# Kernel tuning notes

Measured on AMD Instinct MI355X. Metric: run time of the kernel, lower is better.

## Reference

```python
import jax, jax.numpy as jnp
import numpy as np

NUM_SAMPLES = 1024


def _cdist(a, b):
    # a, b: (n, 3) -> (n, n) pairwise euclidean distances (torch.cdist p=2)
    d2 = jnp.sum((a[:, None, :] - b[None, :, :]) ** 2, axis=-1)
    return jnp.sqrt(jnp.maximum(d2, 0.0))


def _greedy_match_cost(cost):
    # Greedy sequential matching: repeatedly take the global argmin over
    # still-unmatched rows/cols, accumulate its cost, eliminate row+col.
    n = cost.shape[0]

    def step(carry, _):
        row_mask, col_mask, loss = carry
        valid = row_mask[:, None] & col_mask[None, :]
        masked = jnp.where(valid, cost, jnp.inf)
        idx = jnp.argmin(masked)  # row-major first-min == torch's min(dim=1)+argmin tiebreak
        r = idx // n
        c = idx % n
        loss = loss + cost[r, c]
        return (row_mask.at[r].set(False), col_mask.at[c].set(False), loss), None

    init = (jnp.ones((n,), dtype=bool), jnp.ones((n,), dtype=bool), jnp.float32(0.0))
    (_, _, loss), _ = jax.lax.scan(step, init, None, length=n)
    return loss / n


def setup_inputs() -> dict:
    key = jax.random.key(0)
    k1, k2, k3 = jax.random.split(key, 3)
    B, N, n = 8, 4096, NUM_SAMPLES
    S1 = jax.random.normal(k1, (B, N, 3), dtype=jnp.float32)
    S2 = jax.random.normal(k2, (B, N, 3), dtype=jnp.float32)
    # torch.randperm(N)[:n] per batch element: without-replacement sampling
    perm_keys = jax.random.split(k3, B)
    indices = jax.vmap(lambda k: jax.random.permutation(k, N)[:n])(perm_keys).astype(jnp.int32)
    return {"S1": S1, "S2": S2, "indices": indices}


def reference(S1, S2, indices):
    # sample the same indices from both sets, per batch (matches original loop)
    s1 = jnp.take_along_axis(S1, indices[:, :, None], axis=1)  # (B, n, 3)
    s2 = jnp.take_along_axis(S2, indices[:, :, None], axis=1)  # (B, n, 3)
    cost = jax.vmap(_cdist)(s1, s2)  # (B, n, n)
    losses = jax.vmap(_greedy_match_cost)(cost)  # (B,)
    return jnp.mean(losses)
```

## Files before the change

### kernel.cpp

```cpp
#include <hip/hip_runtime.h>
#include <stdint.h>

#define BATCH 8
#define NPTS 4096
#define NS 1024
#define KD 6

typedef unsigned long long u64;
typedef unsigned int u32;
typedef unsigned short u16;
typedef unsigned char u8;

#define DEADV (~0ull)
#define QNANB 0x7FC00000u
#define INFB  0x7F800000u

__device__ __forceinline__ float pdist3(float ax, float ay, float az,
                                        float bx, float by, float bz) {
    float dx = ax - bx, dy = ay - by, dz = az - bz;
    float d2 = __fmaf_rn(dz, dz, __fmaf_rn(dy, dy, dx * dx));
    return __fsqrt_rn(d2);
}

__device__ __forceinline__ u64 packv(float d, u32 row, u32 col) {
    return ((u64)__float_as_uint(d) << 20) | ((u64)row << 10) | (u64)col;
}

__device__ __forceinline__ u64 u64min2(u64 a, u64 b) { return a < b ? a : b; }

__device__ __forceinline__ u64 tree16(const u64* p) {
    u64 a0 = u64min2(p[0], p[1]),   a1 = u64min2(p[2], p[3]);
    u64 a2 = u64min2(p[4], p[5]),   a3 = u64min2(p[6], p[7]);
    u64 a4 = u64min2(p[8], p[9]),   a5 = u64min2(p[10], p[11]);
    u64 a6 = u64min2(p[12], p[13]), a7 = u64min2(p[14], p[15]);
    u64 b0 = u64min2(a0, a1), b1 = u64min2(a2, a3);
    u64 b2 = u64min2(a4, a5), b3 = u64min2(a6, a7);
    return u64min2(u64min2(b0, b1), u64min2(b2, b3));
}

template<int CTRL>
__device__ __forceinline__ u64 dpp_min_step(u64 m) {
    u32 lo = (u32)m, hi = (u32)(m >> 32);
    u32 olo = (u32)__builtin_amdgcn_update_dpp(-1, (int)lo, CTRL, 0xF, 0xF, false);
    u32 ohi = (u32)__builtin_amdgcn_update_dpp(-1, (int)hi, CTRL, 0xF, 0xF, false);
    u64 o = ((u64)ohi << 32) | olo;
    return o < m ? o : m;
}

__device__ __forceinline__ u64 wave_min_u64(u64 m) {
    m = dpp_min_step<0x111>(m);
    m = dpp_min_step<0x112>(m);
    m = dpp_min_step<0x114>(m);
    m = dpp_min_step<0x118>(m);
    m = dpp_min_step<0x142>(m);
    m = dpp_min_step<0x143>(m);
    u32 lo = (u32)__builtin_amdgcn_readlane((int)(u32)m, 63);
    u32 hi = (u32)__builtin_amdgcn_readlane((int)(u32)(m >> 32), 63);
    return ((u64)hi << 32) | lo;
}

__global__ void gather_k(const float* __restrict__ S1, const float* __restrict__ S2,
                         const int* __restrict__ idx,
                         float4* __restrict__ s1g, float4* __restrict__ s2g,
                         int* __restrict__ cnt) {
    int t = blockIdx.x * blockDim.x + threadIdx.x;
    if (t == 0) *cnt = 0;
    if (t >= BATCH * NS) return;
    int b = t >> 10;
    int j = idx[t];
    const float* p1 = S1 + ((size_t)b * NPTS + j) * 3;
    const float* p2 = S2 + ((size_t)b * NPTS + j) * 3;
    s1g[t] = make_float4(p1[0], p1[1], p1[2], 0.f);
    s2g[t] = make_float4(p2[0], p2[1], p2[2], 0.f);
}

__global__ void lists_k(const float4* __restrict__ s1g, const float4* __restrict__ s2g,
                        u64* __restrict__ rlist_g, u64* __restrict__ clist_g) {
    __shared__ float4 pts[NS];
    int gg = blockIdx.x * 4 + (threadIdx.x >> 6);
    int lane = threadIdx.x & 63;
    int side = (gg >= BATCH * NS) ? 1 : 0;
    int g = gg - side * (BATCH * NS);
    int b = g >> 10;
    u32 rc = (u32)(g & 1023);
    const float4* other = (side ? s1g : s2g) + (size_t)b * NS;
    for (int i = threadIdx.x; i < NS; i += 256) pts[i] = other[i];
    float4 a = side ? s2g[g] : s1g[g];
    __syncthreads();
    u64 cand[16];
    #pragma unroll
    for (int k = 0; k < 16; ++k) {
        int o = lane + (k << 6);
        float4 q = pts[o];
        float d = pdist3(a.x, a.y, a.z, q.x, q.y, q.z);
        cand[k] = side ? packv(d, (u32)o, rc) : packv(d, rc, (u32)o);
    }
    u64* out = (side ? clist_g : rlist_g) + (size_t)g * KD;
    for (int i = 0; i < KD; ++i) {
        u64 m1 = wave_min_u64(tree16(cand));
        if (lane == 0) out[i] = m1;
        #pragma unroll
        for (int k = 0; k < 16; ++k) cand[k] = (cand[k] == m1) ? DEADV : cand[k];
    }
}

__global__ void __launch_bounds__(1024, 1)
resolve_k(const float4* __restrict__ s1g, const float4* __restrict__ s2g,
          const u64* __restrict__ rlist_gl, const u64* __restrict__ clist_gl,
          float* __restrict__ loss_ws, int* __restrict__ cnt,
          float* __restrict__ out) {
    __shared__ u64 rlist[NS * KD];
    __shared__ u64 clist[NS * KD];
    __shared__ u64 rmin[NS];
    __shared__ u64 cmin[NS];
    __shared__ float4 s1p[NS];
    __shared__ float4 s2p[NS];
    __shared__ u8 rptrs[NS], cptrs[NS];
    __shared__ u16 qrow[NS], qcol[NS];
    __shared__ u16 lrows[NS], lcols[NS];
    __shared__ float lred[1024];
    __shared__ int wcntr[16], wcntc[16];
    __shared__ int qrn, qcn, matched, stale_n;
    int b = blockIdx.x;
    int tid = threadIdx.x;
    int lane = tid & 63, wv = tid >> 6;

    {
        const float4* rs = (const float4*)(rlist_gl + (size_t)b * NS * KD);
        const float4* cs = (const float4*)(clist_gl + (size_t)b * NS * KD);
        float4* rd = (float4*)rlist;
        float4* cd = (float4*)clist;
        for (int i = tid; i < NS * KD / 2; i += 1024) { rd[i] = rs[i]; cd[i] = cs[i]; }
    }
    s1p[tid] = s1g[(size_t)b * NS + tid];
    s2p[tid] = s2g[(size_t)b * NS + tid];
    rptrs[tid] = 1; cptrs[tid] = 1;
    lrows[tid] = (u16)tid; lcols[tid] = (u16)tid;
    if (tid == 0) { matched = 0; stale_n = NS; }
    __syncthreads();
    rmin[tid] = rlist[tid * KD];
    cmin[tid] = clist[tid * KD];
    float loss = 0.f;
    __syncthreads();

    for (int round = 0; round < NS; ++round) {
        u64 myk = rmin[tid];
        u32 c = (u32)myk & 1023u;
        bool mut = (myk != DEADV) && (cmin[c] == myk);
        __syncthreads();
        if (mut) {
            loss += __uint_as_float((u32)(myk >> 20));
            rmin[tid] = DEADV;
            cmin[c] = DEADV;
            s1p[tid].x = __uint_as_float(QNANB);
            s2p[c].x   = __uint_as_float(QNANB);
        }
        u64 bal = __ballot((int)mut);
        if (lane == 0 && bal) atomicAdd(&matched, (int)__popcll(bal));
        if (tid == 0) { qrn = 0; qcn = 0; }
        __syncthreads();
        int m = matched;
        if (m >= NS) break;
        int live = NS - m;
        int stale = stale_n;
        bool rebuild = (stale * 4 > live * 5 + 64);
        u64 rk = rmin[tid];
        if (rk != DEADV) {
            float pr = s2p[(u32)rk & 1023u].x;
            if (pr != pr) {
                u32 p = rptrs[tid];
                bool found = false;
                while (p < KD) {
                    u64 e = rlist[tid * KD + p];
                    ++p;
                    if (e != DEADV) {
                        float q = s2p[(u32)e & 1023u].x;
                        if (q == q) { rmin[tid] = e; found = true; break; }
                    }
                }
                rptrs[tid] = (u8)p;
                if (!found) { int s = atomicAdd(&qrn, 1); qrow[s] = (u16)tid; }
            }
        }
        u64 ck = cmin[tid];
        if (ck != DEADV) {
            float pr = s1p[((u32)ck >> 10) & 1023u].x;
            if (pr != pr) {
                u32 p = cptrs[tid];
                bool found = false;
                while (p < KD) {
                    u64 e = clist[tid * KD + p];
                    ++p;
                    if (e != DEADV) {
                        float q = s1p[((u32)e >> 10) & 1023u].x;
                        if (q == q) { cmin[tid] = e; found = true; break; }
                    }
                }
                cptrs[tid] = (u8)p;
                if (!found) { int s = atomicAdd(&qcn, 1); qcol[s] = (u16)tid; }
            }
        }
        if (rebuild) {
            float cx = s2p[tid].x;  bool calive = (cx == cx);
            float rx = s1p[tid].x;  bool ralive = (rx == rx);
            u64 cb = __ballot((int)calive);
            u64 rb = __ballot((int)ralive);
            if (lane == 0) { wcntc[wv] = (int)__popcll(cb); wcntr[wv] = (int)__popcll(rb); }
            __syncthreads();
            int cbase = 0, rbase = 0;
            for (int j = 0; j < wv; ++j) { cbase += wcntc[j]; rbase += wcntr[j]; }
            int crank = (int)__popcll(cb & ((1ull << lane) - 1ull));
            int rrank = (int)__popcll(rb & ((1ull << lane) - 1ull));
            if (calive) lcols[cbase + crank] = (u16)tid;
            if (ralive) lrows[rbase + rrank] = (u16)tid;
        }
        __syncthreads();
        int nr = qrn, nc = qcn;
        int scan_n = rebuild ? live : stale;
        if (rebuild && tid == 0) stale_n = live;
        int tot = nr + nc;
        for (int qi = wv; qi < tot; qi += 16) {
            if (qi < nr) {
                u32 r = qrow[qi];
                float4 a = s1p[r];
                float a1d = __uint_as_float(INFB), a2d = a1d;
                u32 a1i = 1023u, a2i = 1023u;
                for (int i = lane; i < scan_n; i += 64) {
                    int cc = lcols[i];
                    float4 q = s2p[cc];
                    float d = pdist3(a.x, a.y, a.z, q.x, q.y, q.z);
                    bool c1 = d < a1d;
                    bool c2 = d < a2d;
                    float td = c2 ? d : a2d;  u32 ti = c2 ? (u32)cc : a2i;
                    a2d = c1 ? a1d : td;      a2i = c1 ? a1i : ti;
                    a1d = c1 ? d : a1d;       a1i = c1 ? (u32)cc : a1i;
                }
                u32 b1 = __float_as_uint(a1d), b2 = __float_as_uint(a2d);
                u64 m1 = (b1 == INFB) ? DEADV : (((u64)b1 << 10) | a1i);
                u64 m2 = (b2 == INFB) ? DEADV : (((u64)b2 << 10) | a2i);
                u64 M1 = wave_min_u64(m1);
                u64 ck2 = (m1 == M1) ? m2 : m1;
                u64 M2 = wave_min_u64(ck2);
                if (lane == 0) {
                    u64 F1 = ((M1 >> 10) << 20) | ((u64)r << 10) | (M1 & 1023u);
                    u64 F2 = (M2 == DEADV) ? DEADV
                           : (((M2 >> 10) << 20) | ((u64)r << 10) | (M2 & 1023u));
                    rmin[r] = F1;
                    rlist[r * KD + KD - 1] = F2;
                    rptrs[r] = KD - 1;
                }
            } else {
                u32 cc = qcol[qi - nr];
                float4 a = s2p[cc];
                float a1d = __uint_as_float(INFB), a2d = a1d;
                u32 a1i = 1023u, a2i = 1023u;
                for (int i = lane; i < scan_n; i += 64) {
                    int r = lrows[i];
                    float4 q = s1p[r];
                    float d = pdist3(q.x, q.y, q.z, a.x, a.y, a.z);
                    bool c1 = d < a1d;
                    bool c2 = d < a2d;
                    float td = c2 ? d : a2d;  u32 ti = c2 ? (u32)r : a2i;
                    a2d = c1 ? a1d : td;      a2i = c1 ? a1i : ti;
                    a1d = c1 ? d : a1d;       a1i = c1 ? (u32)r : a1i;
                }
                u32 b1 = __float_as_uint(a1d), b2 = __float_as_uint(a2d);
                u64 m1 = (b1 == INFB) ? DEADV : (((u64)b1 << 10) | a1i);
                u64 m2 = (b2 == INFB) ? DEADV : (((u64)b2 << 10) | a2i);
                u64 M1 = wave_min_u64(m1);
                u64 ck2 = (m1 == M1) ? m2 : m1;
                u64 M2 = wave_min_u64(ck2);
                if (lane == 0) {
                    u64 F1 = ((M1 >> 10) << 20) | ((M1 & 1023u) << 10) | (u64)cc;
                    u64 F2 = (M2 == DEADV) ? DEADV
                           : (((M2 >> 10) << 20) | ((M2 & 1023u) << 10) | (u64)cc);
                    cmin[cc] = F1;
                    clist[cc * KD + KD - 1] = F2;
                    cptrs[cc] = KD - 1;
                }
            }
        }
        __syncthreads();
    }

    lred[tid] = loss;
    __syncthreads();
    #pragma unroll
    for (int s = 512; s > 0; s >>= 1) {
        if (tid < s) lred[tid] += lred[tid + s];
        __syncthreads();
    }
    if (tid == 0) {
        atomicExch(&loss_ws[b], lred[0] * (1.0f / NS));
        __threadfence();
        int old = atomicAdd(cnt, 1);
        if (old == BATCH - 1) {
            __threadfence();
            float s = 0.f;
            for (int i = 0; i < BATCH; ++i) s += atomicAdd(&loss_ws[i], 0.0f);
            out[0] = s * (1.0f / BATCH);
        }
    }
}

extern "C" void kernel_launch(void* const* d_in, const int* in_sizes, int n_in,
                              void* d_out, int out_size, void* d_ws, size_t ws_size,
                              hipStream_t stream) {
    const float* S1 = (const float*)d_in[0];
    const float* S2 = (const float*)d_in[1];
    const int* idx  = (const int*)d_in[2];
    char* ws = (char*)d_ws;
    size_t o = 0;
    float4* s1g    = (float4*)(ws + o); o += (size_t)BATCH * NS * 16;
    float4* s2g    = (float4*)(ws + o); o += (size_t)BATCH * NS * 16;
    u64* rlist_g   = (u64*)(ws + o);    o += (size_t)BATCH * NS * KD * 8;
    u64* clist_g   = (u64*)(ws + o);    o += (size_t)BATCH * NS * KD * 8;
    float* loss_ws = (float*)(ws + o);  o += (size_t)BATCH * 4;
    int* cnt       = (int*)(ws + o);

    gather_k<<<(BATCH * NS + 255) / 256, 256, 0, stream>>>(S1, S2, idx, s1g, s2g, cnt);
    lists_k<<<2 * BATCH * NS / 4, 256, 0, stream>>>(s1g, s2g, rlist_g, clist_g);
    resolve_k<<<BATCH, 1024, 0, stream>>>(s1g, s2g, rlist_g, clist_g, loss_ws, cnt,
                                          (float*)d_out);
}
```

Baseline: 201.0 us.

## Compact live point coordinates in place and track liveness with bitmasks

Replaces the index-list indirection (lcols/lrows into s1p/s2p) with compacted coordinate arrays that store the original index in the w lane, so the rescan loop reads contiguous float4s without a gather. Liveness moves to per-side bitmasks, and pos arrays map each original index to its compacted slot. The rescan loops are unrolled and lred now aliases rlist to free shared memory. The compaction in the rebuild step reads and writes the same array within one phase, which adds a possible ordering hazard between threads, and the lred alias assumes rlist is no longer needed when the reduction runs.

```diff
diff --git a/kernel.cpp b/kernel.cpp
--- a/kernel.cpp
+++ b/kernel.cpp
@@ -113,14 +113,15 @@
     __shared__ u64 clist[NS * KD];
     __shared__ u64 rmin[NS];
     __shared__ u64 cmin[NS];
-    __shared__ float4 s1p[NS];
-    __shared__ float4 s2p[NS];
+    __shared__ float4 s1c[NS];
+    __shared__ float4 s2c[NS];
+    __shared__ u16 pos1[NS], pos2[NS];
+    __shared__ u32 am1[NS / 32], am2[NS / 32];
     __shared__ u8 rptrs[NS], cptrs[NS];
     __shared__ u16 qrow[NS], qcol[NS];
-    __shared__ u16 lrows[NS], lcols[NS];
-    __shared__ float lred[1024];
     __shared__ int wcntr[16], wcntc[16];
     __shared__ int qrn, qcn, matched, stale_n;
+    float* lred = (float*)rlist;
     int b = blockIdx.x;
     int tid = threadIdx.x;
     int lane = tid & 63, wv = tid >> 6;
@@ -132,10 +133,15 @@
         float4* cd = (float4*)clist;
         for (int i = tid; i < NS * KD / 2; i += 1024) { rd[i] = rs[i]; cd[i] = cs[i]; }
     }
-    s1p[tid] = s1g[(size_t)b * NS + tid];
-    s2p[tid] = s2g[(size_t)b * NS + tid];
+    {
+        float4 v1 = s1g[(size_t)b * NS + tid]; v1.w = __uint_as_float((u32)tid);
+        s1c[tid] = v1;
+        float4 v2 = s2g[(size_t)b * NS + tid]; v2.w = __uint_as_float((u32)tid);
+        s2c[tid] = v2;
+    }
+    pos1[tid] = (u16)tid; pos2[tid] = (u16)tid;
     rptrs[tid] = 1; cptrs[tid] = 1;
-    lrows[tid] = (u16)tid; lcols[tid] = (u16)tid;
+    if (tid < NS / 32) { am1[tid] = ~0u; am2[tid] = ~0u; }
     if (tid == 0) { matched = 0; stale_n = NS; }
     __syncthreads();
     rmin[tid] = rlist[tid * KD];
@@ -143,6 +149,9 @@
     float loss = 0.f;
     __syncthreads();
 
+#define ALIVE1(i) ((am1[(u32)(i) >> 5] >> ((u32)(i) & 31u)) & 1u)
+#define ALIVE2(i) ((am2[(u32)(i) >> 5] >> ((u32)(i) & 31u)) & 1u)
+
     for (int round = 0; round < NS; ++round) {
         u64 myk = rmin[tid];
         u32 c = (u32)myk & 1023u;
@@ -152,8 +161,10 @@
             loss += __uint_as_float((u32)(myk >> 20));
             rmin[tid] = DEADV;
             cmin[c] = DEADV;
-            s1p[tid].x = __uint_as_float(QNANB);
-            s2p[c].x   = __uint_as_float(QNANB);
+            atomicAnd(&am1[tid >> 5], ~(1u << (tid & 31)));
+            atomicAnd(&am2[c >> 5],   ~(1u << (c & 31)));
+            s1c[pos1[tid]].x = __uint_as_float(QNANB);
+            s2c[pos2[c]].x   = __uint_as_float(QNANB);
         }
         u64 bal = __ballot((int)mut);
         if (lane == 0 && bal) atomicAdd(&matched, (int)__popcll(bal));
@@ -166,16 +177,14 @@
         bool rebuild = (stale * 4 > live * 5 + 64);
         u64 rk = rmin[tid];
         if (rk != DEADV) {
-            float pr = s2p[(u32)rk & 1023u].x;
-            if (pr != pr) {
+            if (!ALIVE2((u32)rk & 1023u)) {
                 u32 p = rptrs[tid];
                 bool found = false;
                 while (p < KD) {
                     u64 e = rlist[tid * KD + p];
                     ++p;
-                    if (e != DEADV) {
-                        float q = s2p[(u32)e & 1023u].x;
-                        if (q == q) { rmin[tid] = e; found = true; break; }
+                    if (e != DEADV && ALIVE2((u32)e & 1023u)) {
+                        rmin[tid] = e; found = true; break;
                     }
                 }
                 rptrs[tid] = (u8)p;
@@ -184,16 +193,14 @@
         }
         u64 ck = cmin[tid];
         if (ck != DEADV) {
-            float pr = s1p[((u32)ck >> 10) & 1023u].x;
-            if (pr != pr) {
+            if (!ALIVE1(((u32)ck >> 10) & 1023u)) {
                 u32 p = cptrs[tid];
                 bool found = false;
                 while (p < KD) {
                     u64 e = clist[tid * KD + p];
                     ++p;
-                    if (e != DEADV) {
-                        float q = s1p[((u32)e >> 10) & 1023u].x;
-                        if (q == q) { cmin[tid] = e; found = true; break; }
+                    if (e != DEADV && ALIVE1(((u32)e >> 10) & 1023u)) {
+                        cmin[tid] = e; found = true; break;
                     }
                 }
                 cptrs[tid] = (u8)p;
@@ -201,8 +208,11 @@
             }
         }
         if (rebuild) {
-            float cx = s2p[tid].x;  bool calive = (cx == cx);
-            float rx = s1p[tid].x;  bool ralive = (rx == rx);
+            bool calive = ALIVE2(tid) != 0u;
+            bool ralive = ALIVE1(tid) != 0u;
+            float4 cv, rv;
+            if (calive) cv = s2c[pos2[tid]];
+            if (ralive) rv = s1c[pos1[tid]];
             u64 cb = __ballot((int)calive);
             u64 rb = __ballot((int)ralive);
             if (lane == 0) { wcntc[wv] = (int)__popcll(cb); wcntr[wv] = (int)__popcll(rb); }
@@ -211,8 +221,8 @@
             for (int j = 0; j < wv; ++j) { cbase += wcntc[j]; rbase += wcntr[j]; }
             int crank = (int)__popcll(cb & ((1ull << lane) - 1ull));
             int rrank = (int)__popcll(rb & ((1ull << lane) - 1ull));
-            if (calive) lcols[cbase + crank] = (u16)tid;
-            if (ralive) lrows[rbase + rrank] = (u16)tid;
+            if (calive) { int np = cbase + crank; pos2[tid] = (u16)np; s2c[np] = cv; }
+            if (ralive) { int np = rbase + rrank; pos1[tid] = (u16)np; s1c[np] = rv; }
         }
         __syncthreads();
         int nr = qrn, nc = qcn;
@@ -222,18 +232,19 @@
         for (int qi = wv; qi < tot; qi += 16) {
             if (qi < nr) {
                 u32 r = qrow[qi];
-                float4 a = s1p[r];
+                float4 a = s1c[pos1[r]];
                 float a1d = __uint_as_float(INFB), a2d = a1d;
                 u32 a1i = 1023u, a2i = 1023u;
+                #pragma unroll 4
                 for (int i = lane; i < scan_n; i += 64) {
-                    int cc = lcols[i];
-                    float4 q = s2p[cc];
+                    float4 q = s2c[i];
                     float d = pdist3(a.x, a.y, a.z, q.x, q.y, q.z);
+                    u32 ci = __float_as_uint(q.w);
                     bool c1 = d < a1d;
                     bool c2 = d < a2d;
-                    float td = c2 ? d : a2d;  u32 ti = c2 ? (u32)cc : a2i;
+                    float td = c2 ? d : a2d;  u32 ti = c2 ? ci : a2i;
                     a2d = c1 ? a1d : td;      a2i = c1 ? a1i : ti;
-                    a1d = c1 ? d : a1d;       a1i = c1 ? (u32)cc : a1i;
+                    a1d = c1 ? d : a1d;       a1i = c1 ? ci : a1i;
                 }
                 u32 b1 = __float_as_uint(a1d), b2 = __float_as_uint(a2d);
                 u64 m1 = (b1 == INFB) ? DEADV : (((u64)b1 << 10) | a1i);
@@ -251,18 +262,19 @@
                 }
             } else {
                 u32 cc = qcol[qi - nr];
-                float4 a = s2p[cc];
+                float4 a = s2c[pos2[cc]];
                 float a1d = __uint_as_float(INFB), a2d = a1d;
                 u32 a1i = 1023u, a2i = 1023u;
+                #pragma unroll 4
                 for (int i = lane; i < scan_n; i += 64) {
-                    int r = lrows[i];
-                    float4 q = s1p[r];
+                    float4 q = s1c[i];
                     float d = pdist3(q.x, q.y, q.z, a.x, a.y, a.z);
+                    u32 ri = __float_as_uint(q.w);
                     bool c1 = d < a1d;
                     bool c2 = d < a2d;
-                    float td = c2 ? d : a2d;  u32 ti = c2 ? (u32)r : a2i;
+                    float td = c2 ? d : a2d;  u32 ti = c2 ? ri : a2i;
                     a2d = c1 ? a1d : td;      a2i = c1 ? a1i : ti;
-                    a1d = c1 ? d : a1d;       a1i = c1 ? (u32)r : a1i;
+                    a1d = c1 ? d : a1d;       a1i = c1 ? ri : a1i;
                 }
                 u32 b1 = __float_as_uint(a1d), b2 = __float_as_uint(a2d);
                 u64 m1 = (b1 == INFB) ? DEADV : (((u64)b1 << 10) | a1i);
```

Result: slower. 205.7 us (+2.4%).
